# Kernel tuning notes

Hardware: AMD Instinct MI355X
Metric: run time of the kernel (lower is better)

Reference implementation:

```python
import jax, jax.numpy as jnp
import numpy as np

N = 800000      # octree nodes at this depth
CIN = 32
COUT = 64
K = 27          # 3x3x3 kernel neighborhood
EPS = 1e-5
GROUPS = COUT // 4


def group_norm(x, w, b, groups=GROUPS, eps=EPS):
    # x: [N, C]; per-node GroupNorm over channel groups (torch GroupNorm on [N, C])
    n, c = x.shape
    xg = x.reshape(n, groups, c // groups)
    mu = jnp.mean(xg, axis=-1, keepdims=True)
    var = jnp.mean(jnp.square(xg - mu), axis=-1, keepdims=True)
    xn = (xg - mu) * jax.lax.rsqrt(var + eps)
    return xn.reshape(n, c) * w + b


def octree_conv(x, neigh, W):
    # x: [N, Cin], neigh: [N, K] int, W: [K, Cin, Cout]
    # out[i] = sum_k x[neigh[i, k]] @ W[k]; fixed small loop over K kernel taps
    out = x[neigh[:, 0]] @ W[0]
    for k in range(1, W.shape[0]):
        out = out + x[neigh[:, k]] @ W[k]
    return out


def setup_inputs() -> dict:
    key = jax.random.key(0)
    ks = jax.random.split(key, 12)
    data = jax.random.normal(ks[0], (N, CIN), jnp.float32)
    neigh = jax.random.randint(ks[1], (N, K), 0, N, dtype=jnp.int64)
    scale_a = 1.0 / np.sqrt(K * CIN)
    scale_b = 1.0 / np.sqrt(K * COUT)
    Wa = jax.random.normal(ks[2], (K, CIN, COUT), jnp.float32) * scale_a
    Wb = jax.random.normal(ks[3], (K, COUT, COUT), jnp.float32) * scale_b
    W1 = jax.random.normal(ks[4], (CIN, COUT), jnp.float32) * (1.0 / np.sqrt(CIN))
    ga_w = 1.0 + 0.1 * jax.random.normal(ks[5], (COUT,), jnp.float32)
    ga_b = 0.01 * jax.random.normal(ks[6], (COUT,), jnp.float32)
    gb_w = 1.0 + 0.1 * jax.random.normal(ks[7], (COUT,), jnp.float32)
    gb_b = 0.01 * jax.random.normal(ks[8], (COUT,), jnp.float32)
    gs_w = 1.0 + 0.1 * jax.random.normal(ks[9], (COUT,), jnp.float32)
    gs_b = 0.01 * jax.random.normal(ks[10], (COUT,), jnp.float32)
    return {"data": data, "neigh": neigh, "Wa": Wa, "ga_w": ga_w, "ga_b": ga_b,
            "Wb": Wb, "gb_w": gb_w, "gb_b": gb_b, "W1": W1, "gs_w": gs_w, "gs_b": gs_b}


def reference(data, neigh, Wa, ga_w, ga_b, Wb, gb_w, gb_b, W1, gs_w, gs_b):
    # conv3x3a: OctreeConv -> GroupNorm -> ReLU
    h = jax.nn.relu(group_norm(octree_conv(data, neigh, Wa), ga_w, ga_b))
    # conv3x3b: OctreeConv -> GroupNorm
    h2 = group_norm(octree_conv(h, neigh, Wb), gb_w, gb_b)
    # shortcut (in_channels != out_channels): Conv1x1 -> GroupNorm
    sc = group_norm(data @ W1, gs_w, gs_b)
    return jax.nn.relu(h2 + sc)
```

## Files before the change

kernel.cpp:

```cpp
#include <hip/hip_runtime.h>

#define NNODES 800000
#define CINC   32
#define COUTC  64
#define KT     27
#define EPSV   1e-5f

typedef _Float16 half8 __attribute__((ext_vector_type(8)));
typedef _Float16 half4 __attribute__((ext_vector_type(4)));
typedef float    f32x4 __attribute__((ext_vector_type(4)));

#define MFMA(A, B, C) __builtin_amdgcn_mfma_f32_16x16x32_f16((A), (B), (C), 0, 0, 0)

__device__ __forceinline__ f32x4 gn4(f32x4 v, const float* __restrict__ w,
                                     const float* __restrict__ b, int cb) {
  const float mu = (v[0] + v[1] + v[2] + v[3]) * 0.25f;
  f32x4 d;
#pragma unroll
  for (int j = 0; j < 4; ++j) d[j] = v[j] - mu;
  const float var = (d[0] * d[0] + d[1] * d[1] + d[2] * d[2] + d[3] * d[3]) * 0.25f;
  const float rs = 1.0f / sqrtf(var + EPSV);
  const f32x4 wv = *(const f32x4*)(w + cb);
  const f32x4 bv = *(const f32x4*)(b + cb);
  f32x4 r;
#pragma unroll
  for (int j = 0; j < 4; ++j) r[j] = d[j] * rs * wv[j] + bv[j];
  return r;
}

__global__ __launch_bounds__(256) void k_split(const float* __restrict__ x,
                                               _Float16* __restrict__ dpk, int n4) {
  const int i = blockIdx.x * 256 + threadIdx.x;
  if (i >= n4) return;
  const f32x4 v = ((const f32x4*)x)[i];
  half4 h, l;
#pragma unroll
  for (int j = 0; j < 4; ++j) {
    h[j] = (_Float16)v[j];
    l[j] = (_Float16)(v[j] - (float)h[j]);
  }
  const int n = i >> 3, g = i & 7;
  *(half4*)(dpk + (size_t)n * 64 + g * 4) = h;
  *(half4*)(dpk + (size_t)n * 64 + 32 + g * 4) = l;
}

__global__ __launch_bounds__(256) void k_prepw(const float* __restrict__ Wa,
                                               const float* __restrict__ Wb,
                                               const float* __restrict__ W1,
                                               _Float16* __restrict__ waT,
                                               _Float16* __restrict__ wbT,
                                               _Float16* __restrict__ w1T) {
  const int u = blockIdx.x * 256 + threadIdx.x;
  const float* s;
  _Float16* d;
  size_t db;
  int cin0, cout;
  if (u < 6912) {
    const int tap = u >> 8, r = u & 255, t = r >> 6, l = r & 63;
    cin0 = (l >> 4) * 8;
    cout = t * 16 + (l & 15);
    s = Wa + (size_t)tap * CINC * COUTC;
    d = waT;
    db = ((size_t)(tap * 8 + t * 2) * 64 + l) * 8;
  } else if (u < 20736) {
    const int u2 = u - 6912;
    const int tap = u2 >> 9, r = u2 & 511, t = r >> 7, r2 = r & 127;
    const int kc = r2 >> 6, l = r2 & 63;
    cin0 = kc * 32 + (l >> 4) * 8;
    cout = t * 16 + (l & 15);
    s = Wb + (size_t)tap * COUTC * COUTC;
    d = wbT;
    db = ((size_t)(tap * 16 + t * 4 + kc * 2) * 64 + l) * 8;
  } else if (u < 20992) {
    const int u3 = u - 20736, t = u3 >> 6, l = u3 & 63;
    cin0 = (l >> 4) * 8;
    cout = t * 16 + (l & 15);
    s = W1;
    d = w1T;
    db = ((size_t)(t * 2) * 64 + l) * 8;
  } else {
    return;
  }
  half8 h, l8;
#pragma unroll
  for (int j = 0; j < 8; ++j) {
    const float v = s[(size_t)(cin0 + j) * COUTC + cout];
    h[j] = (_Float16)v;
    l8[j] = (_Float16)(v - (float)h[j]);
  }
  *(half8*)(d + db) = h;
  *(half8*)(d + db + 512) = l8;
}

__global__ __launch_bounds__(256, 4) void k_conva(
    const _Float16* __restrict__ dpk, const int* __restrict__ neigh,
    const _Float16* __restrict__ waT, const float* __restrict__ gw,
    const float* __restrict__ gb, _Float16* __restrict__ hpk) {
  __shared__ int s_n[128 * KT];
  const int tid = threadIdx.x;
  const int wave = tid >> 6, lane = tid & 63;
  const int cl = lane & 15, q = lane >> 4;
  const int node0 = blockIdx.x * 128;

  for (int j = tid; j < 128 * KT; j += 256) s_n[j] = neigh[(size_t)node0 * KT + j];
  __syncthreads();

  f32x4 acc[4][2] = {};
  const int ln0 = wave * 32 + cl;
  const _Float16* wp = waT + lane * 8;

  auto gath = [&](int tap, half8& xh0, half8& xl0, half8& xh1, half8& xl1) {
    const int i0 = s_n[ln0 * KT + tap];
    const int i1 = s_n[(ln0 + 16) * KT + tap];
    const _Float16* p0 = dpk + (size_t)i0 * 64 + q * 8;
    const _Float16* p1 = dpk + (size_t)i1 * 64 + q * 8;
    xh0 = *(const half8*)(p0);
    xl0 = *(const half8*)(p0 + 32);
    xh1 = *(const half8*)(p1);
    xl1 = *(const half8*)(p1 + 32);
  };
  auto comp = [&](int tap, half8 xh0, half8 xl0, half8 xh1, half8 xl1) {
#pragma unroll
    for (int t = 0; t < 4; ++t) {
      const half8 wh = *(const half8*)(wp + (size_t)(tap * 8 + t * 2) * 512);
      const half8 wl = *(const half8*)(wp + (size_t)(tap * 8 + t * 2) * 512 + 512);
      acc[t][0] = MFMA(wh, xh0, acc[t][0]);
      acc[t][0] = MFMA(wh, xl0, acc[t][0]);
      acc[t][0] = MFMA(wl, xh0, acc[t][0]);
      acc[t][1] = MFMA(wh, xh1, acc[t][1]);
      acc[t][1] = MFMA(wh, xl1, acc[t][1]);
      acc[t][1] = MFMA(wl, xh1, acc[t][1]);
    }
  };

  half8 a0h, a0l, a1h, a1l, b0h, b0l, b1h, b1l;
  gath(0, a0h, a0l, a1h, a1l);
  for (int tap = 0; tap < KT; tap += 2) {
    if (tap + 1 < KT) gath(tap + 1, b0h, b0l, b1h, b1l);
    comp(tap, a0h, a0l, a1h, a1l);
    if (tap + 2 < KT) gath(tap + 2, a0h, a0l, a1h, a1l);
    if (tap + 1 < KT) comp(tap + 1, b0h, b0l, b1h, b1l);
  }

#pragma unroll
  for (int t = 0; t < 4; ++t)
#pragma unroll
    for (int nt = 0; nt < 2; ++nt) {
      const int node = node0 + wave * 32 + nt * 16 + cl;
      const int cb = t * 16 + q * 4;
      const f32x4 g = gn4(acc[t][nt], gw, gb, cb);
      half4 h, l;
#pragma unroll
      for (int j = 0; j < 4; ++j) {
        const float v = fmaxf(g[j], 0.0f);
        h[j] = (_Float16)v;
        l[j] = (_Float16)(v - (float)h[j]);
      }
      *(half4*)(hpk + (size_t)node * 128 + cb) = h;
      *(half4*)(hpk + (size_t)node * 128 + 64 + cb) = l;
    }
}

__global__ __launch_bounds__(256, 3) void k_convb(
    const _Float16* __restrict__ hpk, const _Float16* __restrict__ dpk,
    const int* __restrict__ neigh, const _Float16* __restrict__ wbT,
    const _Float16* __restrict__ w1T,
    const float* __restrict__ gbw, const float* __restrict__ gbb,
    const float* __restrict__ gsw, const float* __restrict__ gsb,
    float* __restrict__ out) {
  __shared__ int s_n[128 * KT];
  const int tid = threadIdx.x;
  const int wave = tid >> 6, lane = tid & 63;
  const int cl = lane & 15, q = lane >> 4;
  const int node0 = blockIdx.x * 128;

  for (int j = tid; j < 128 * KT; j += 256) s_n[j] = neigh[(size_t)node0 * KT + j];
  __syncthreads();

  f32x4 acc[4][2] = {};
  const int ln0 = wave * 32 + cl;
  const _Float16* wp = wbT + lane * 8;

  auto gath = [&](int tap, half8& h0a, half8& h0b, half8& l0a, half8& l0b,
                  half8& h1a, half8& h1b, half8& l1a, half8& l1b) {
    const int i0 = s_n[ln0 * KT + tap];
    const int i1 = s_n[(ln0 + 16) * KT + tap];
    const _Float16* p0 = hpk + (size_t)i0 * 128 + q * 8;
    const _Float16* p1 = hpk + (size_t)i1 * 128 + q * 8;
    h0a = *(const half8*)(p0);
    h0b = *(const half8*)(p0 + 32);
    l0a = *(const half8*)(p0 + 64);
    l0b = *(const half8*)(p0 + 96);
    h1a = *(const half8*)(p1);
    h1b = *(const half8*)(p1 + 32);
    l1a = *(const half8*)(p1 + 64);
    l1b = *(const half8*)(p1 + 96);
  };
  auto comp = [&](int tap, half8 h0a, half8 h0b, half8 l0a, half8 l0b,
                  half8 h1a, half8 h1b, half8 l1a, half8 l1b) {
#pragma unroll
    for (int t = 0; t < 4; ++t) {
      const _Float16* wb0 = wp + (size_t)(tap * 16 + t * 4) * 512;
      const half8 wha = *(const half8*)(wb0);
      const half8 wla = *(const half8*)(wb0 + 512);
      const half8 whb = *(const half8*)(wb0 + 1024);
      const half8 wlb = *(const half8*)(wb0 + 1536);
      acc[t][0] = MFMA(wha, h0a, acc[t][0]);
      acc[t][0] = MFMA(wha, l0a, acc[t][0]);
      acc[t][0] = MFMA(wla, h0a, acc[t][0]);
      acc[t][0] = MFMA(whb, h0b, acc[t][0]);
      acc[t][0] = MFMA(whb, l0b, acc[t][0]);
      acc[t][0] = MFMA(wlb, h0b, acc[t][0]);
      acc[t][1] = MFMA(wha, h1a, acc[t][1]);
      acc[t][1] = MFMA(wha, l1a, acc[t][1]);
      acc[t][1] = MFMA(wla, h1a, acc[t][1]);
      acc[t][1] = MFMA(whb, h1b, acc[t][1]);
      acc[t][1] = MFMA(whb, l1b, acc[t][1]);
      acc[t][1] = MFMA(wlb, h1b, acc[t][1]);
    }
  };

  half8 a0, a1, a2, a3, a4, a5, a6, a7;
  half8 b0, b1, b2, b3, b4, b5, b6, b7;
  gath(0, a0, a1, a2, a3, a4, a5, a6, a7);
  for (int tap = 0; tap < KT; tap += 2) {
    if (tap + 1 < KT) gath(tap + 1, b0, b1, b2, b3, b4, b5, b6, b7);
    comp(tap, a0, a1, a2, a3, a4, a5, a6, a7);
    if (tap + 2 < KT) gath(tap + 2, a0, a1, a2, a3, a4, a5, a6, a7);
    if (tap + 1 < KT) comp(tap + 1, b0, b1, b2, b3, b4, b5, b6, b7);
  }

  f32x4 sc[4][2] = {};
  {
    const int n0g = node0 + wave * 32 + cl;
    const _Float16* p0 = dpk + (size_t)n0g * 64 + q * 8;
    const _Float16* p1 = dpk + (size_t)(n0g + 16) * 64 + q * 8;
    const half8 sh0 = *(const half8*)(p0);
    const half8 sl0 = *(const half8*)(p0 + 32);
    const half8 sh1 = *(const half8*)(p1);
    const half8 sl1 = *(const half8*)(p1 + 32);
    const _Float16* w1p = w1T + lane * 8;
#pragma unroll
    for (int t = 0; t < 4; ++t) {
      const half8 wh = *(const half8*)(w1p + (size_t)(t * 2) * 512);
      const half8 wl = *(const half8*)(w1p + (size_t)(t * 2) * 512 + 512);
      sc[t][0] = MFMA(wh, sh0, sc[t][0]);
      sc[t][0] = MFMA(wh, sl0, sc[t][0]);
      sc[t][0] = MFMA(wl, sh0, sc[t][0]);
      sc[t][1] = MFMA(wh, sh1, sc[t][1]);
      sc[t][1] = MFMA(wh, sl1, sc[t][1]);
      sc[t][1] = MFMA(wl, sh1, sc[t][1]);
    }
  }

#pragma unroll
  for (int t = 0; t < 4; ++t)
#pragma unroll
    for (int nt = 0; nt < 2; ++nt) {
      const int node = node0 + wave * 32 + nt * 16 + cl;
      const int cb = t * 16 + q * 4;
      const f32x4 a = gn4(acc[t][nt], gbw, gbb, cb);
      const f32x4 s = gn4(sc[t][nt], gsw, gsb, cb);
      f32x4 o;
#pragma unroll
      for (int j = 0; j < 4; ++j) o[j] = fmaxf(a[j] + s[j], 0.0f);
      *(f32x4*)(out + (size_t)node * 64 + cb) = o;
    }
}

extern "C" void kernel_launch(void* const* d_in, const int* in_sizes, int n_in,
                              void* d_out, int out_size, void* d_ws, size_t ws_size,
                              hipStream_t stream) {
  const float* data = (const float*)d_in[0];
  const int* neigh = (const int*)d_in[1];
  const float* Wa = (const float*)d_in[2];
  const float* gaw = (const float*)d_in[3];
  const float* gab = (const float*)d_in[4];
  const float* Wb = (const float*)d_in[5];
  const float* gbw = (const float*)d_in[6];
  const float* gbb = (const float*)d_in[7];
  const float* W1 = (const float*)d_in[8];
  const float* gsw = (const float*)d_in[9];
  const float* gsb = (const float*)d_in[10];
  float* out = (float*)d_out;

  char* ws = (char*)d_ws;
  _Float16* dpk = (_Float16*)(ws);
  _Float16* hpk = (_Float16*)(ws + 102400000);
  _Float16* waT = (_Float16*)(ws + 307200000);
  _Float16* wbT = (_Float16*)(ws + 307421184);
  _Float16* w1T = (_Float16*)(ws + 307863552);

  k_split<<<25000, 256, 0, stream>>>(data, dpk, NNODES * CINC / 4);
  k_prepw<<<82, 256, 0, stream>>>(Wa, Wb, W1, waT, wbT, w1T);

  k_conva<<<NNODES / 128, 256, 0, stream>>>(dpk, neigh, waT, gaw, gab, hpk);

  k_convb<<<NNODES / 128, 256, 0, stream>>>(hpk, dpk, neigh, wbT, w1T,
                                            gbw, gbb, gsw, gsb, out);
}
```

Before: 1.913 ms.

## Stage per-tap weights into LDS via async loads with triple-buffered gathers

In both conv kernels, each tap's weight slice is now copied cooperatively into a double-buffered LDS tile with global_load_lds, and the MFMAs read weights from LDS instead of each wave loading them from global memory. The neighbor-feature gathers move to a three-deep register rotation, with explicit vmcnt waits and two block barriers per tap. The aim is to cut redundant global/L2 weight traffic and overlap the gather latency with compute. The cost is extra barriers per tap, more LDS per block, which may lower occupancy, and more live registers. The hand-counted vmcnt values must match the issued loads exactly.

After: 1.606 ms. 16.0% less time.

```diff
diff --git a/kernel.cpp b/kernel.cpp
--- a/kernel.cpp
+++ b/kernel.cpp
@@ -11,6 +11,14 @@
 typedef float    f32x4 __attribute__((ext_vector_type(4)));
 
 #define MFMA(A, B, C) __builtin_amdgcn_mfma_f32_16x16x32_f16((A), (B), (C), 0, 0, 0)
+#define SBAR()  __builtin_amdgcn_s_barrier()
+#define SCHED() __builtin_amdgcn_sched_barrier(0)
+
+__device__ __forceinline__ void gl2lds(const _Float16* g, _Float16* l) {
+  __builtin_amdgcn_global_load_lds(
+      (const __attribute__((address_space(1))) void*)g,
+      (__attribute__((address_space(3))) void*)l, 16, 0, 0);
+}
 
 __device__ __forceinline__ f32x4 gn4(f32x4 v, const float* __restrict__ w,
                                      const float* __restrict__ b, int cb) {
@@ -92,11 +100,56 @@
   *(half8*)(d + db + 512) = l8;
 }
 
+#define STAGEA(T, SL)                                                          \
+  {                                                                            \
+    const _Float16* sp_ = waT + (size_t)(T)*4096 + (wave * 2) * 512 + lane * 8;\
+    _Float16* dp_ = s_w + (SL)*4096 + (wave * 2) * 512;                        \
+    gl2lds(sp_, dp_);                                                          \
+    gl2lds(sp_ + 512, dp_ + 512);                                              \
+  }
+
+#define GATHA(T, GB)                                                           \
+  {                                                                            \
+    const int i0_ = s_n[ln0 * KT + (T)];                                       \
+    const int i1_ = s_n[(ln0 + 16) * KT + (T)];                                \
+    const _Float16* p0_ = dpk + (size_t)i0_ * 64 + q * 8;                      \
+    const _Float16* p1_ = dpk + (size_t)i1_ * 64 + q * 8;                      \
+    GB[0] = *(const half8*)(p0_);                                              \
+    GB[1] = *(const half8*)(p0_ + 32);                                         \
+    GB[2] = *(const half8*)(p1_);                                              \
+    GB[3] = *(const half8*)(p1_ + 32);                                         \
+  }
+
+#define STEPA(T, S, GBC, GBN, VMS, DOSTAGE, DOG)                               \
+  {                                                                            \
+    SCHED();                                                                   \
+    SBAR();                           \
+    SCHED();                                                                   \
+    if (DOSTAGE) STAGEA((T) + 1, 1 - (S));                                     \
+    if (DOG) GATHA((T) + 2, GBN);                                              \
+    asm volatile("s_waitcnt vmcnt(" VMS ")" ::: "memory");                     \
+    SCHED();                                                                   \
+    SBAR();                         \
+    SCHED();                                                                   \
+    _Pragma("unroll") for (int t4 = 0; t4 < 4; ++t4) {                         \
+      const _Float16* wb_ = s_w + (S)*4096 + (t4 * 2) * 512 + lane * 8;        \
+      const half8 wh_ = *(const half8*)(wb_);                                  \
+      const half8 wl_ = *(const half8*)(wb_ + 512);                            \
+      acc[t4][0] = MFMA(wh_, GBC[0], acc[t4][0]);                              \
+      acc[t4][0] = MFMA(wh_, GBC[1], acc[t4][0]);                              \
+      acc[t4][0] = MFMA(wl_, GBC[0], acc[t4][0]);                              \
+      acc[t4][1] = MFMA(wh_, GBC[2], acc[t4][1]);                              \
+      acc[t4][1] = MFMA(wh_, GBC[3], acc[t4][1]);                              \
+      acc[t4][1] = MFMA(wl_, GBC[2], acc[t4][1]);                              \
+    }                                                                          \
+  }
+
 __global__ __launch_bounds__(256, 4) void k_conva(
     const _Float16* __restrict__ dpk, const int* __restrict__ neigh,
     const _Float16* __restrict__ waT, const float* __restrict__ gw,
     const float* __restrict__ gb, _Float16* __restrict__ hpk) {
   __shared__ int s_n[128 * KT];
+  __shared__ _Float16 s_w[2 * 4096];
   const int tid = threadIdx.x;
   const int wave = tid >> 6, lane = tid & 63;
   const int cl = lane & 15, q = lane >> 4;
@@ -107,40 +160,23 @@
 
   f32x4 acc[4][2] = {};
   const int ln0 = wave * 32 + cl;
-  const _Float16* wp = waT + lane * 8;
-
-  auto gath = [&](int tap, half8& xh0, half8& xl0, half8& xh1, half8& xl1) {
-    const int i0 = s_n[ln0 * KT + tap];
-    const int i1 = s_n[(ln0 + 16) * KT + tap];
-    const _Float16* p0 = dpk + (size_t)i0 * 64 + q * 8;
-    const _Float16* p1 = dpk + (size_t)i1 * 64 + q * 8;
-    xh0 = *(const half8*)(p0);
-    xl0 = *(const half8*)(p0 + 32);
-    xh1 = *(const half8*)(p1);
-    xl1 = *(const half8*)(p1 + 32);
-  };
-  auto comp = [&](int tap, half8 xh0, half8 xl0, half8 xh1, half8 xl1) {
-#pragma unroll
-    for (int t = 0; t < 4; ++t) {
-      const half8 wh = *(const half8*)(wp + (size_t)(tap * 8 + t * 2) * 512);
-      const half8 wl = *(const half8*)(wp + (size_t)(tap * 8 + t * 2) * 512 + 512);
-      acc[t][0] = MFMA(wh, xh0, acc[t][0]);
-      acc[t][0] = MFMA(wh, xl0, acc[t][0]);
-      acc[t][0] = MFMA(wl, xh0, acc[t][0]);
-      acc[t][1] = MFMA(wh, xh1, acc[t][1]);
-      acc[t][1] = MFMA(wh, xl1, acc[t][1]);
-      acc[t][1] = MFMA(wl, xh1, acc[t][1]);
-    }
-  };
-
-  half8 a0h, a0l, a1h, a1l, b0h, b0l, b1h, b1l;
-  gath(0, a0h, a0l, a1h, a1l);
-  for (int tap = 0; tap < KT; tap += 2) {
-    if (tap + 1 < KT) gath(tap + 1, b0h, b0l, b1h, b1l);
-    comp(tap, a0h, a0l, a1h, a1l);
-    if (tap + 2 < KT) gath(tap + 2, a0h, a0l, a1h, a1l);
-    if (tap + 1 < KT) comp(tap + 1, b0h, b0l, b1h, b1l);
-  }
+  half8 g0[4], g1[4], g2[4];
+
+  STAGEA(0, 0);
+  GATHA(0, g0);
+  GATHA(1, g1);
+
+  for (int c6 = 0; c6 < 24; c6 += 6) {
+    STEPA(c6 + 0, 0, g0, g2, "10", 1, 1);
+    STEPA(c6 + 1, 1, g1, g0, "10", 1, 1);
+    STEPA(c6 + 2, 0, g2, g1, "10", 1, 1);
+    STEPA(c6 + 3, 1, g0, g2, "10", 1, 1);
+    STEPA(c6 + 4, 0, g1, g0, "10", 1, 1);
+    STEPA(c6 + 5, 1, g2, g1, "10", 1, 1);
+  }
+  STEPA(24, 0, g0, g2, "10", 1, 1);
+  STEPA(25, 1, g1, g0, "6", 1, 0);
+  STEPA(26, 0, g2, g1, "0", 0, 0);
 
 #pragma unroll
   for (int t = 0; t < 4; ++t)
@@ -161,6 +197,64 @@
     }
 }
 
+#define STAGEB(T, SL)                                                          \
+  {                                                                            \
+    const _Float16* sp_ = wbT + (size_t)(T)*8192 + (wave * 4) * 512 + lane * 8;\
+    _Float16* dp_ = s_w + (SL)*8192 + (wave * 4) * 512;                        \
+    gl2lds(sp_, dp_);                                                          \
+    gl2lds(sp_ + 512, dp_ + 512);                                              \
+    gl2lds(sp_ + 1024, dp_ + 1024);                                            \
+    gl2lds(sp_ + 1536, dp_ + 1536);                                            \
+  }
+
+#define GATHB(T, GB)                                                           \
+  {                                                                            \
+    const int i0_ = s_n[ln0 * KT + (T)];                                       \
+    const int i1_ = s_n[(ln0 + 16) * KT + (T)];                                \
+    const _Float16* p0_ = hpk + (size_t)i0_ * 128 + q * 8;                     \
+    const _Float16* p1_ = hpk + (size_t)i1_ * 128 + q * 8;                     \
+    GB[0] = *(const half8*)(p0_);                                              \
+    GB[1] = *(const half8*)(p0_ + 32);                                         \
+    GB[2] = *(const half8*)(p0_ + 64);                                         \
+    GB[3] = *(const half8*)(p0_ + 96);                                         \
+    GB[4] = *(const half8*)(p1_);                                              \
+    GB[5] = *(const half8*)(p1_ + 32);                                         \
+    GB[6] = *(const half8*)(p1_ + 64);                                         \
+    GB[7] = *(const half8*)(p1_ + 96);                                         \
+  }
+
+#define STEPB(T, S, GBC, GBN, VMS, DOSTAGE, DOG)                               \
+  {                                                                            \
+    SCHED();                                                                   \
+    SBAR();                                                                    \
+    SCHED();                                                                   \
+    if (DOSTAGE) STAGEB((T) + 1, 1 - (S));                                     \
+    if (DOG) GATHB((T) + 2, GBN);                                              \
+    asm volatile("s_waitcnt vmcnt(" VMS ")" ::: "memory");                     \
+    SCHED();                                                                   \
+    SBAR();                                                                    \
+    SCHED();                                                                   \
+    _Pragma("unroll") for (int t4 = 0; t4 < 4; ++t4) {                         \
+      const _Float16* wb_ = s_w + (S)*8192 + (t4 * 4) * 512 + lane * 8;        \
+      const half8 wha_ = *(const half8*)(wb_);                                 \
+      const half8 wla_ = *(const half8*)(wb_ + 512);                           \
+      const half8 whb_ = *(const half8*)(wb_ + 1024);                          \
+      const half8 wlb_ = *(const half8*)(wb_ + 1536);                          \
+      acc[t4][0] = MFMA(wha_, GBC[0], acc[t4][0]);                             \
+      acc[t4][0] = MFMA(wha_, GBC[2], acc[t4][0]);                             \
+      acc[t4][0] = MFMA(wla_, GBC[0], acc[t4][0]);                             \
+      acc[t4][0] = MFMA(whb_, GBC[1], acc[t4][0]);                             \
+      acc[t4][0] = MFMA(whb_, GBC[3], acc[t4][0]);                             \
+      acc[t4][0] = MFMA(wlb_, GBC[1], acc[t4][0]);                             \
+      acc[t4][1] = MFMA(wha_, GBC[4], acc[t4][1]);                             \
+      acc[t4][1] = MFMA(wha_, GBC[6], acc[t4][1]);                             \
+      acc[t4][1] = MFMA(wla_, GBC[4], acc[t4][1]);                             \
+      acc[t4][1] = MFMA(whb_, GBC[5], acc[t4][1]);                             \
+      acc[t4][1] = MFMA(whb_, GBC[7], acc[t4][1]);                             \
+      acc[t4][1] = MFMA(wlb_, GBC[5], acc[t4][1]);                             \
+    }                                                                          \
+  }
+
 __global__ __launch_bounds__(256, 3) void k_convb(
     const _Float16* __restrict__ hpk, const _Float16* __restrict__ dpk,
     const int* __restrict__ neigh, const _Float16* __restrict__ wbT,
@@ -169,6 +263,7 @@
     const float* __restrict__ gsw, const float* __restrict__ gsb,
     float* __restrict__ out) {
   __shared__ int s_n[128 * KT];
+  __shared__ _Float16 s_w[2 * 8192];
   const int tid = threadIdx.x;
   const int wave = tid >> 6, lane = tid & 63;
   const int cl = lane & 15, q = lane >> 4;
@@ -179,56 +274,23 @@
 
   f32x4 acc[4][2] = {};
   const int ln0 = wave * 32 + cl;
-  const _Float16* wp = wbT + lane * 8;
-
-  auto gath = [&](int tap, half8& h0a, half8& h0b, half8& l0a, half8& l0b,
-                  half8& h1a, half8& h1b, half8& l1a, half8& l1b) {
-    const int i0 = s_n[ln0 * KT + tap];
-    const int i1 = s_n[(ln0 + 16) * KT + tap];
-    const _Float16* p0 = hpk + (size_t)i0 * 128 + q * 8;
-    const _Float16* p1 = hpk + (size_t)i1 * 128 + q * 8;
-    h0a = *(const half8*)(p0);
-    h0b = *(const half8*)(p0 + 32);
-    l0a = *(const half8*)(p0 + 64);
-    l0b = *(const half8*)(p0 + 96);
-    h1a = *(const half8*)(p1);
-    h1b = *(const half8*)(p1 + 32);
-    l1a = *(const half8*)(p1 + 64);
-    l1b = *(const half8*)(p1 + 96);
-  };
-  auto comp = [&](int tap, half8 h0a, half8 h0b, half8 l0a, half8 l0b,
-                  half8 h1a, half8 h1b, half8 l1a, half8 l1b) {
-#pragma unroll
-    for (int t = 0; t < 4; ++t) {
-      const _Float16* wb0 = wp + (size_t)(tap * 16 + t * 4) * 512;
-      const half8 wha = *(const half8*)(wb0);
-      const half8 wla = *(const half8*)(wb0 + 512);
-      const half8 whb = *(const half8*)(wb0 + 1024);
-      const half8 wlb = *(const half8*)(wb0 + 1536);
-      acc[t][0] = MFMA(wha, h0a, acc[t][0]);
-      acc[t][0] = MFMA(wha, l0a, acc[t][0]);
-      acc[t][0] = MFMA(wla, h0a, acc[t][0]);
-      acc[t][0] = MFMA(whb, h0b, acc[t][0]);
-      acc[t][0] = MFMA(whb, l0b, acc[t][0]);
-      acc[t][0] = MFMA(wlb, h0b, acc[t][0]);
-      acc[t][1] = MFMA(wha, h1a, acc[t][1]);
-      acc[t][1] = MFMA(wha, l1a, acc[t][1]);
-      acc[t][1] = MFMA(wla, h1a, acc[t][1]);
-      acc[t][1] = MFMA(whb, h1b, acc[t][1]);
-      acc[t][1] = MFMA(whb, l1b, acc[t][1]);
-      acc[t][1] = MFMA(wlb, h1b, acc[t][1]);
-    }
-  };
-
-  half8 a0, a1, a2, a3, a4, a5, a6, a7;
-  half8 b0, b1, b2, b3, b4, b5, b6, b7;
-  gath(0, a0, a1, a2, a3, a4, a5, a6, a7);
-  for (int tap = 0; tap < KT; tap += 2) {
-    if (tap + 1 < KT) gath(tap + 1, b0, b1, b2, b3, b4, b5, b6, b7);
-    comp(tap, a0, a1, a2, a3, a4, a5, a6, a7);
-    if (tap + 2 < KT) gath(tap + 2, a0, a1, a2, a3, a4, a5, a6, a7);
-    if (tap + 1 < KT) comp(tap + 1, b0, b1, b2, b3, b4, b5, b6, b7);
-  }
+  half8 g0[8], g1[8], g2[8];
+
+  STAGEB(0, 0);
+  GATHB(0, g0);
+  GATHB(1, g1);
+
+  for (int c6 = 0; c6 < 24; c6 += 6) {
+    STEPB(c6 + 0, 0, g0, g2, "20", 1, 1);
+    STEPB(c6 + 1, 1, g1, g0, "20", 1, 1);
+    STEPB(c6 + 2, 0, g2, g1, "20", 1, 1);
+    STEPB(c6 + 3, 1, g0, g2, "20", 1, 1);
+    STEPB(c6 + 4, 0, g1, g0, "20", 1, 1);
+    STEPB(c6 + 5, 1, g2, g1, "20", 1, 1);
+  }
+  STEPB(24, 0, g0, g2, "20", 1, 1);
+  STEPB(25, 1, g1, g0, "12", 1, 0);
+  STEPB(26, 0, g2, g1, "0", 0, 0);
 
   f32x4 sc[4][2] = {};
   {
@@ -295,7 +357,6 @@
   k_prepw<<<82, 256, 0, stream>>>(Wa, Wb, W1, waT, wbT, w1T);
 
   k_conva<<<NNODES / 128, 256, 0, stream>>>(dpk, neigh, waT, gaw, gab, hpk);
-
   k_convb<<<NNODES / 128, 256, 0, stream>>>(hpk, dpk, neigh, wbT, w1T,
                                             gbw, gbb, gsw, gsb, out);
 }
```
